# Optimization experiments

Measured on AMD Instinct MI355X. Metric: run time of the kernel, lower is better.

The kernel has to match this reference:

```python
import jax, jax.numpy as jnp
import numpy as np
from jax import lax

EPS = 1e-8

def int8_fq(x):
    # Int8ActPerTensorFloat: per-tensor float scale from runtime max-abs, fake-quant with STE.
    s = jnp.maximum(jnp.max(jnp.abs(x)) / 127.0, EPS)
    q = jnp.clip(jnp.round(x / s), -128.0, 127.0) * s
    return x + lax.stop_gradient(q - x)

def bin_w(w):
    # BINARY weight quant: per-tensor scale = mean(|w|), weights -> +/- scale (STE).
    s = jnp.mean(jnp.abs(w))
    wq = jnp.where(w >= 0, s, -s)
    return w + lax.stop_gradient(wq - w)

def qrelu(x):
    # QuantReLU with int8 input_quant and int8 act_quant
    return int8_fq(jax.nn.relu(int8_fq(x)))

def conv2d(x, w, b):
    y = lax.conv_general_dilated(x, w, window_strides=(1, 1), padding='VALID',
                                 dimension_numbers=('NCHW', 'OIHW', 'NCHW'))
    return y + b[None, :, None, None]

def maxpool2(x):
    return lax.reduce_window(x, -jnp.inf, lax.max, (1, 1, 2, 2), (1, 1, 2, 2), 'VALID')

def setup_inputs() -> dict:
    key = jax.random.key(0)
    ks = jax.random.split(key, 12)
    B = 16384
    inp = {
        'input_tensor': jax.random.normal(ks[0], (B, 3, 32, 32), dtype=jnp.float32),
        'w1': jax.random.normal(ks[1], (6, 3, 5, 5), dtype=jnp.float32) * 0.1,
        'b1': jax.random.normal(ks[2], (6,), dtype=jnp.float32) * 0.01,
        'w2': jax.random.normal(ks[3], (16, 6, 5, 5), dtype=jnp.float32) * 0.1,
        'b2': jax.random.normal(ks[4], (16,), dtype=jnp.float32) * 0.01,
        'fw1': jax.random.normal(ks[5], (120, 400), dtype=jnp.float32) * 0.05,
        'fb1': jax.random.normal(ks[6], (120,), dtype=jnp.float32) * 0.01,
        'fw2': jax.random.normal(ks[7], (84, 120), dtype=jnp.float32) * 0.05,
        'fb2': jax.random.normal(ks[8], (84,), dtype=jnp.float32) * 0.01,
        'fw3': jax.random.normal(ks[9], (10, 84), dtype=jnp.float32) * 0.05,
        'fb3': jax.random.normal(ks[10], (10,), dtype=jnp.float32) * 0.01,
    }
    return inp

def reference(input_tensor, w1, b1, w2, b2, fw1, fb1, fw2, fb2, fw3, fb3):
    x = int8_fq(input_tensor)                  # QuantIdentity
    x = qrelu(conv2d(x, bin_w(w1), b1))        # conv1 + relu1: [B,6,28,28]
    x = maxpool2(x)                            # [B,6,14,14]
    x = qrelu(conv2d(x, bin_w(w2), b2))        # conv2 + relu2: [B,16,10,10]
    x = maxpool2(x)                            # [B,16,5,5]
    x = x.reshape(x.shape[0], -1)              # [B,400]
    x = qrelu(x @ bin_w(fw1).T + fb1)          # fc1 + relu3: [B,120]
    x = qrelu(x @ bin_w(fw2).T + fb2)          # fc2 + relu4: [B,84]
    out = x @ bin_w(fw3).T + fb3               # fc3: [B,10]
    return out
```

## Files before the change

kernel.cpp:

```cpp
#include <hip/hip_runtime.h>
#include <math.h>

#define BATCH 16384
#define EPSQ 1e-8f

#define OFF_SCAL 0
#define OFF_WPK1 16
#define OFF_WPK2 196
#define OFF_FQ1  1156
#define OFF_FQ2  13156
#define OFF_FQ3  15844
#define OFF_A    16384
#define OFF_QIN   OFF_A
#define OFF_QC2   OFF_A
#define OFF_ISUM2 (OFF_A + 6400000)
#define OFF_QC3   (OFF_A + 10000000)
#define OFF_P3    (OFF_A + 12000000)
#define OFF_P4    (OFF_A + 14000000)
#define OFF_ISUM1 (OFF_A + 18874368)

__device__ inline int sdot4(unsigned int a, unsigned int b, int c) {
    return __builtin_amdgcn_sdot4((int)a, (int)b, c, false);
}

__device__ inline unsigned int fkey(float f) {
    unsigned int u = __float_as_uint(f);
    return (u & 0x80000000u) ? ~u : (u | 0x80000000u);
}
__device__ inline float fdec(unsigned int k) {
    unsigned int u = (k & 0x80000000u) ? (k ^ 0x80000000u) : ~k;
    return __uint_as_float(u);
}
#define KEY_ZERO   0x80000000u
#define KEY_NEGINF 0x007FFFFFu

__device__ inline float waveMax(float v) {
    #pragma unroll
    for (int off = 32; off > 0; off >>= 1)
        v = fmaxf(v, __shfl_down(v, off, 64));
    return v;
}

__device__ inline void blockAtomicMax2(float vmax, float vnmax,
                                       unsigned int* gmax, unsigned int* gnmax) {
    __shared__ float sm[4], sn[4];
    float a = waveMax(vmax), b = waveMax(vnmax);
    int tid = threadIdx.x;
    if ((tid & 63) == 0) { sm[tid >> 6] = a; sn[tid >> 6] = b; }
    __syncthreads();
    if (tid == 0) {
        atomicMax(gmax, fkey(fmaxf(fmaxf(sm[0], sm[1]), fmaxf(sm[2], sm[3]))));
        atomicMax(gnmax, fkey(fmaxf(fmaxf(sn[0], sn[1]), fmaxf(sn[2], sn[3]))));
    }
}

__device__ inline float fq_elem(float x, float s) {
    float q = fminf(fmaxf(rintf(x / s), -128.0f), 127.0f);
    return q * s;
}
__device__ inline int qrelu_code(float x, float s1, float s2) {
    float q = fq_elem(x, s1);
    q = fmaxf(q, 0.0f);
    return (int)fminf(fmaxf(rintf(q / s2), -128.0f), 127.0f);
}
__device__ inline void get_qrelu_scales(const unsigned int* scalu, int slot,
                                        float& s1, float& s2) {
    float maxa = fdec(scalu[slot]), negm = fdec(scalu[slot + 1]);
    float absm = fmaxf(maxa, negm);
    s1 = fmaxf(absm / 127.0f, EPSQ);
    float qm = fminf(fmaxf(rintf(maxa / s1), -128.0f), 127.0f) * s1;
    s2 = fmaxf(fmaxf(qm, 0.0f) / 127.0f, EPSQ);
}

__device__ inline unsigned int sgn8(float w) { return (w >= 0.0f) ? 0x01u : 0xFFu; }

__device__ inline unsigned int u32at(const unsigned int* wv, int wi, int k) {
    return (k == 0) ? wv[wi]
        : __builtin_amdgcn_perm(wv[wi + 1], wv[wi], 0x03020100u + 0x01010101u * (unsigned)k);
}

__global__ __launch_bounds__(256) void prep_kernel(const float* __restrict__ w1,
        const float* __restrict__ w2, const float* __restrict__ fw1,
        const float* __restrict__ fw2, const float* __restrict__ fw3,
        float* __restrict__ wsf) {
    int blk = blockIdx.x, tid = threadIdx.x;
    unsigned int* wsu = (unsigned int*)wsf;
    if (blk == 0) {
        if (tid == 0) wsu[0] = KEY_ZERO;
        else if (tid <= 8) wsu[tid] = KEY_NEGINF;
        return;
    }
    const float* src = nullptr; int N = 0;
    if (blk == 1)      { src = w1;  N = 450; }
    else if (blk == 2) { src = w2;  N = 2400; }
    else if (blk == 3) { src = fw1; N = 48000; }
    else if (blk == 4) { src = fw2; N = 10080; }
    else               { src = fw3; N = 840; }
    __shared__ float red[256];
    float partial = 0.0f;
    for (int i = tid; i < N; i += 256) partial += fabsf(src[i]);
    red[tid] = partial;
    __syncthreads();
    for (int s = 128; s > 0; s >>= 1) {
        if (tid < s) red[tid] += red[tid + s];
        __syncthreads();
    }
    if (tid == 0) wsf[8 + blk] = red[0] / (float)N;

    if (blk == 1) {
        for (int t = tid; t < 90; t += 256) {
            const float* wp = w1 + t * 5;
            wsu[OFF_WPK1 + 2*t] = sgn8(wp[0]) | (sgn8(wp[1])<<8) | (sgn8(wp[2])<<16) | (sgn8(wp[3])<<24);
            wsu[OFF_WPK1 + 2*t + 1] = sgn8(wp[4]) << 24;
        }
    } else if (blk == 2) {
        for (int t = tid; t < 480; t += 256) {
            const float* wp = w2 + t * 5;
            wsu[OFF_WPK2 + 2*t] = sgn8(wp[0]) | (sgn8(wp[1])<<8) | (sgn8(wp[2])<<16) | (sgn8(wp[3])<<24);
            wsu[OFF_WPK2 + 2*t + 1] = sgn8(wp[4]) << 24;
        }
    } else if (blk == 3) {
        for (int i = tid; i < 12000; i += 256) {
            int j = i / 100, k = i % 100;
            const float* wp = fw1 + j * 400 + k * 4;
            wsu[OFF_FQ1 + i] = sgn8(wp[0]) | (sgn8(wp[1])<<8) | (sgn8(wp[2])<<16) | (sgn8(wp[3])<<24);
        }
    } else if (blk == 4) {
        for (int i = tid; i < 2688; i += 256) {
            int j = i >> 5, k = i & 31;
            unsigned int u = 0;
            if (k < 30) {
                const float* wp = fw2 + j * 120 + k * 4;
                u = sgn8(wp[0]) | (sgn8(wp[1])<<8) | (sgn8(wp[2])<<16) | (sgn8(wp[3])<<24);
            }
            wsu[OFF_FQ2 + i] = u;
        }
    } else {
        for (int i = tid; i < 240; i += 256) {
            int j = i / 24, k = i % 24;
            unsigned int u = 0;
            if (k < 21) {
                const float* wp = fw3 + j * 84 + k * 4;
                u = sgn8(wp[0]) | (sgn8(wp[1])<<8) | (sgn8(wp[2])<<16) | (sgn8(wp[3])<<24);
            }
            wsu[OFF_FQ3 + i] = u;
        }
    }
}

__global__ __launch_bounds__(256) void absmax_kernel(const float4* __restrict__ x, int n4,
                                                     unsigned int* __restrict__ gkey) {
    float m = 0.0f;
    int stride = gridDim.x * 256;
    for (int i = blockIdx.x * 256 + threadIdx.x; i < n4; i += stride) {
        float4 v = x[i];
        m = fmaxf(m, fmaxf(fmaxf(fabsf(v.x), fabsf(v.y)), fmaxf(fabsf(v.z), fabsf(v.w))));
    }
    __shared__ float sm[4];
    m = waveMax(m);
    int tid = threadIdx.x;
    if ((tid & 63) == 0) sm[tid >> 6] = m;
    __syncthreads();
    if (tid == 0)
        atomicMax(gkey, fkey(fmaxf(fmaxf(sm[0], sm[1]), fmaxf(sm[2], sm[3]))));
}

__global__ __launch_bounds__(256) void quant1_kernel(const float4* __restrict__ x,
                                                     float* __restrict__ wsf) {
    unsigned int* wsu = (unsigned int*)wsf;
    float s0 = fmaxf(fdec(wsu[0]) / 127.0f, EPSQ);
    unsigned int* qin = wsu + OFF_QIN;
    int stride = gridDim.x * 256;
    const int total = BATCH * 96 * 12;
    for (int unit = blockIdx.x * 256 + threadIdx.x; unit < total; unit += stride) {
        int row_id = unit / 12, w = unit % 12;
        int plane = row_id >> 5, row = row_id & 31;
        int slot = (row >> 1) + ((row & 1) << 4);
        unsigned int u = 0;
        if (w < 8) {
            float4 v = x[row_id * 8 + w];
            int q0 = (int)fminf(fmaxf(rintf(v.x / s0), -128.f), 127.f);
            int q1 = (int)fminf(fmaxf(rintf(v.y / s0), -128.f), 127.f);
            int q2 = (int)fminf(fmaxf(rintf(v.z / s0), -128.f), 127.f);
            int q3 = (int)fminf(fmaxf(rintf(v.w / s0), -128.f), 127.f);
            u = (q0 & 255) | ((q1 & 255) << 8) | ((q2 & 255) << 16) | ((unsigned)(q3 & 255) << 24);
        }
        qin[(plane * 32 + slot) * 12 + w] = u;
    }
}

#define C1_ROWP 48
#define C1_CIS  1536
#define C1_IMGS 4608
#define C1_NIMG 8

template<int PH>
__device__ __forceinline__ void c1_phase(const unsigned char* ib, const unsigned int* wcp,
                                         int* ip, int& gmax, int& gmin) {
    int a0[14], a1[14];
    #pragma unroll
    for (int i = 0; i < 14; i++) { a0[i] = 0; a1[i] = 0; }
    #pragma unroll 1
    for (int ci = 0; ci < 3; ci++) {
        uint4 A[6]; unsigned int Bv[6];
        const unsigned char* cb = ib + ci * C1_CIS;
        #pragma unroll
        for (int r = 0; r < 6; r++) {
            const unsigned char* rb = cb + (((r & 1) << 4) + (r >> 1)) * C1_ROWP;
            if (PH == 0) {
                A[r]  = *(const uint4*)(rb);
                Bv[r] = *(const unsigned int*)(rb + 16);
            } else {
                Bv[r] = *(const unsigned int*)(rb + 12);
                A[r]  = *(const uint4*)(rb + 16);
            }
        }
        const unsigned int* wkp = wcp + ci * 10;
        unsigned int wk0[5], wk4[5];
        #pragma unroll
        for (int ky = 0; ky < 5; ky++) { wk0[ky] = wkp[2*ky]; wk4[ky] = wkp[2*ky+1]; }
        #pragma unroll
        for (int r6 = 0; r6 < 6; r6++) {
            unsigned int wq[5];
            if (PH == 0) {
                wq[0] = A[r6].x; wq[1] = A[r6].y; wq[2] = A[r6].z; wq[3] = A[r6].w; wq[4] = Bv[r6];
            } else {
                wq[0] = __builtin_amdgcn_perm(A[r6].x, Bv[r6],  0x05040302u);
                wq[1] = __builtin_amdgcn_perm(A[r6].y, A[r6].x, 0x05040302u);
                wq[2] = __builtin_amdgcn_perm(A[r6].z, A[r6].y, 0x05040302u);
                wq[3] = __builtin_amdgcn_perm(A[r6].w, A[r6].z, 0x05040302u);
                wq[4] = __builtin_amdgcn_perm(A[r6].w, A[r6].w, 0x00000302u);
            }
            unsigned int up[15];
            #pragma unroll
            for (int i = 0; i < 15; i++) up[i] = u32at(wq, i >> 2, i & 3);
            if (r6 <= 4) {
                unsigned int w0 = wk0[r6], w4 = wk4[r6];
                #pragma unroll
                for (int i = 0; i < 14; i++) {
                    a0[i] = sdot4(up[i], w0, a0[i]);
                    a0[i] = sdot4(up[i+1], w4, a0[i]);
                }
            }
            if (r6 >= 1) {
                unsigned int w0 = wk0[r6-1], w4 = wk4[r6-1];
                #pragma unroll
                for (int i = 0; i < 14; i++) {
                    a1[i] = sdot4(up[i], w0, a1[i]);
                    a1[i] = sdot4(up[i+1], w4, a1[i]);
                }
            }
        }
    }
    #pragma unroll
    for (int i = 0; i < 14; i++) {
        gmax = max(gmax, max(a0[i], a1[i]));
        gmin = min(gmin, min(a0[i], a1[i]));
    }
    #pragma unroll
    for (int p = 0; p < 7; p++)
        ip[p] = max(max(a0[2*p], a0[2*p+1]), max(a1[2*p], a1[2*p+1]));
}

__global__ __launch_bounds__(256) void conv1_kernel(const float* __restrict__ b1,
                                                    float* __restrict__ wsf) {
    __shared__ __align__(16) unsigned char xq[C1_NIMG * C1_IMGS];
    __shared__ unsigned int wpk[180];
    __shared__ float bsm[6];
    unsigned int* wsu = (unsigned int*)wsf;
    int tid = threadIdx.x;
    int b0 = blockIdx.x * C1_NIMG;
    float s0 = fmaxf(fdec(wsu[0]) / 127.0f, EPSQ);
    float seff = s0 * wsf[9];

    {
        const uint4* src = (const uint4*)((const unsigned char*)(wsu + OFF_QIN) + (size_t)b0 * C1_IMGS);
        uint4* dst = (uint4*)xq;
        for (int i = tid; i < C1_NIMG * 288; i += 256) dst[i] = src[i];
    }
    for (int i = tid; i < 180; i += 256) wpk[i] = wsu[OFF_WPK1 + i];
    if (tid < 6) bsm[tid] = b1[tid];
    __syncthreads();

    unsigned int* isum1 = wsu + OFF_ISUM1;
    float vmax = -INFINITY, vnmax = -INFINITY;
    const int ntask = C1_NIMG * 84;
    for (int t = tid; t < ntask; t += 256) {
        int img = t / 84, r = t % 84;
        int c = r / 14, py = r % 14;
        const unsigned char* ib = &xq[img * C1_IMGS + py * C1_ROWP];
        const unsigned int* wcp = &wpk[c * 30];
        int ip0[7], ip1[7];
        int gmax = -2000000000, gmin = 2000000000;
        c1_phase<0>(ib, wcp, ip0, gmax, gmin);
        c1_phase<1>(ib, wcp, ip1, gmax, gmin);
        float bias = bsm[c];
        vmax  = fmaxf(vmax,  fmaf(seff, (float)gmax, bias));
        vnmax = fmaxf(vnmax, -fmaf(seff, (float)gmin, bias));
        unsigned int* dst = isum1 + 588 * (size_t)(b0 + img) + 7 * (c * 14 + py);
        int v14[14];
        #pragma unroll
        for (int p = 0; p < 7; p++) { v14[p] = ip0[p]; v14[7 + p] = ip1[p]; }
        #pragma unroll
        for (int p = 0; p < 7; p++)
            dst[p] = (v14[2*p] & 0xFFFF) | ((unsigned)(v14[2*p+1] & 0xFFFF) << 16);
    }
    blockAtomicMax2(vmax, vnmax, wsu + 1, wsu + 2);
}

__global__ __launch_bounds__(256) void quant2_kernel(const float* __restrict__ b1,
                                                     float* __restrict__ wsf) {
    unsigned int* wsu = (unsigned int*)wsf;
    float s1, s2;
    get_qrelu_scales(wsu, 1, s1, s2);
    float s0 = fmaxf(fdec(wsu[0]) / 127.0f, EPSQ);
    float seff = s0 * wsf[9];
    float bv[6];
    #pragma unroll
    for (int c = 0; c < 6; c++) bv[c] = b1[c];
    const short* isum1 = (const short*)(wsu + OFF_ISUM1);
    unsigned int* qc2 = wsu + OFF_QC2;
    int stride = gridDim.x * 256;
    const int total = BATCH * 84 * 4;
    for (int unit = blockIdx.x * 256 + threadIdx.x; unit < total; unit += stride) {
        int row_id = unit >> 2, w = unit & 3;
        int bci = row_id / 14, row = row_id % 14;
        int ci = bci % 6;
        int slot = (row >> 1) + ((row & 1) << 3);
        float bias = bv[ci];
        unsigned int u = 0;
        const short* sp = isum1 + (size_t)bci * 196 + row * 14;
        #pragma unroll
        for (int k = 0; k < 4; k++) {
            int col = w * 4 + k;
            int code = 0;
            if (col < 14) {
                float pre = fmaf(seff, (float)sp[col], bias);
                code = qrelu_code(pre, s1, s2);
            }
            u |= ((unsigned)(code & 255)) << (8 * k);
        }
        qc2[((size_t)bci * 16 + slot) * 4 + w] = u;
    }
}

#define C2_ROWP 16
#define C2_CIS  256
#define C2_IMGS 1536
#define C2_NIMG 12

__global__ __launch_bounds__(256) void conv2_kernel(const float* __restrict__ b2,
                                                    float* __restrict__ wsf) {
    __shared__ __align__(16) unsigned char act[C2_NIMG * C2_IMGS];
    __shared__ unsigned int wpk[960];
    __shared__ float bsm[16];
    __shared__ __align__(16) short spb[C2_NIMG * 400];
    unsigned int* wsu = (unsigned int*)wsf;
    int tid = threadIdx.x;
    int b0 = blockIdx.x * C2_NIMG;
    int nimg = min(C2_NIMG, BATCH - b0);
    float s1, s2;
    get_qrelu_scales(wsu, 1, s1, s2);
    float seff = s2 * wsf[10];

    {
        const uint4* src = (const uint4*)((const unsigned char*)(wsu + OFF_QC2) + (size_t)b0 * C2_IMGS);
        uint4* dst = (uint4*)act;
        for (int i = tid; i < nimg * 96; i += 256) dst[i] = src[i];
    }
    for (int i = tid; i < 960; i += 256) wpk[i] = wsu[OFF_WPK2 + i];
    if (tid < 16) bsm[tid] = b2[tid];
    __syncthreads();

    float vmax = -INFINITY, vnmax = -INFINITY;
    int ntask = nimg * 80;
    for (int t = tid; t < ntask; t += 256) {
        int img = t / 80, r = t % 80;
        int c = r / 5, py = r % 5;
        const unsigned char* ib = &act[img * C2_IMGS + py * C2_ROWP];
        int a0[10], a1[10];
        #pragma unroll
        for (int i = 0; i < 10; i++) { a0[i] = 0; a1[i] = 0; }
        #pragma unroll 1
        for (int cig = 0; cig < 3; cig++) {
            uint4 R[2][6];
            #pragma unroll
            for (int g = 0; g < 2; g++)
                #pragma unroll
                for (int r6 = 0; r6 < 6; r6++)
                    R[g][r6] = *(const uint4*)(ib + (2*cig + g) * C2_CIS
                                + (((r6 & 1) << 3) + (r6 >> 1)) * C2_ROWP);
            #pragma unroll
            for (int g = 0; g < 2; g++) {
                int ci = 2*cig + g;
                const unsigned int* wkp = &wpk[(c * 6 + ci) * 10];
                unsigned int wk0[5], wk4[5];
                #pragma unroll
                for (int ky = 0; ky < 5; ky++) { wk0[ky] = wkp[2*ky]; wk4[ky] = wkp[2*ky+1]; }
                #pragma unroll
                for (int r6 = 0; r6 < 6; r6++) {
                    unsigned int wv[4] = { R[g][r6].x, R[g][r6].y, R[g][r6].z, R[g][r6].w };
                    unsigned int up[11];
                    #pragma unroll
                    for (int i = 0; i < 11; i++) up[i] = u32at(wv, i >> 2, i & 3);
                    if (r6 <= 4) {
                        unsigned int w0 = wk0[r6], w4 = wk4[r6];
                        #pragma unroll
                        for (int i = 0; i < 10; i++) {
                            a0[i] = sdot4(up[i], w0, a0[i]);
                            a0[i] = sdot4(up[i+1], w4, a0[i]);
                        }
                    }
                    if (r6 >= 1) {
                        unsigned int w0 = wk0[r6-1], w4 = wk4[r6-1];
                        #pragma unroll
                        for (int i = 0; i < 10; i++) {
                            a1[i] = sdot4(up[i], w0, a1[i]);
                            a1[i] = sdot4(up[i+1], w4, a1[i]);
                        }
                    }
                }
            }
        }
        int gmax = -2000000000, gmin = 2000000000;
        #pragma unroll
        for (int i = 0; i < 10; i++) {
            gmax = max(gmax, max(a0[i], a1[i]));
            gmin = min(gmin, min(a0[i], a1[i]));
        }
        float bias = bsm[c];
        vmax  = fmaxf(vmax,  fmaf(seff, (float)gmax, bias));
        vnmax = fmaxf(vnmax, -fmaf(seff, (float)gmin, bias));
        short* dst = spb + img * 400 + c * 25 + py * 5;
        #pragma unroll
        for (int p = 0; p < 5; p++)
            dst[p] = (short)max(max(a0[2*p], a0[2*p+1]), max(a1[2*p], a1[2*p+1]));
    }
    __syncthreads();
    {
        const uint4* pb4 = (const uint4*)spb;
        uint4* d4 = (uint4*)((short*)(wsu + OFF_ISUM2) + (size_t)b0 * 400);
        for (int i = tid; i < nimg * 50; i += 256) d4[i] = pb4[i];
    }
    blockAtomicMax2(vmax, vnmax, wsu + 3, wsu + 4);
}

__global__ __launch_bounds__(256) void quant3_kernel(const float* __restrict__ b2,
                                                     float* __restrict__ wsf) {
    unsigned int* wsu = (unsigned int*)wsf;
    float s1, s2;
    get_qrelu_scales(wsu, 3, s1, s2);
    float sp1, sp2;
    get_qrelu_scales(wsu, 1, sp1, sp2);
    float seff = sp2 * wsf[10];
    __shared__ float bv[16];
    if (threadIdx.x < 16) bv[threadIdx.x] = b2[threadIdx.x];
    __syncthreads();
    const short* isum2 = (const short*)(wsu + OFF_ISUM2);
    unsigned int* qc3 = wsu + OFF_QC3;
    int stride = gridDim.x * 256;
    const int total = BATCH * 100;
    for (int unit = blockIdx.x * 256 + threadIdx.x; unit < total; unit += stride) {
        int b = unit / 100, w = unit % 100;
        const short* sp = isum2 + (size_t)b * 400 + w * 4;
        unsigned int u = 0;
        #pragma unroll
        for (int k = 0; k < 4; k++) {
            int p = w * 4 + k;
            float pre = fmaf(seff, (float)sp[k], bv[p / 25]);
            int code = qrelu_code(pre, s1, s2);
            u |= ((unsigned)(code & 255)) << (8 * k);
        }
        qc3[unit] = u;
    }
}

__global__ __launch_bounds__(256) void fc1_kernel(const float* __restrict__ fb1,
                                                  float* __restrict__ wsf) {
    __shared__ unsigned int xs[32][100];
    __shared__ __align__(16) float pb[32 * 120];
    unsigned int* wsu = (unsigned int*)wsf;
    float* p3 = wsf + OFF_P3;
    int tid = threadIdx.x;
    size_t row0 = (size_t)blockIdx.x * 32;
    float s1, s2;
    get_qrelu_scales(wsu, 3, s1, s2);
    float seff = s2 * wsf[11];
    {
        const uint4* src = (const uint4*)(wsu + OFF_QC3 + row0 * 100);
        uint4* dst = (uint4*)xs;
        for (int i = tid; i < 800; i += 256) dst[i] = src[i];
    }
    __syncthreads();
    float vmax = -INFINITY, vnmax = -INFINITY;
    if (tid < 240) {
        int g = tid / 120, j = tid % 120;
        int acc[16];
        #pragma unroll
        for (int r = 0; r < 16; r++) acc[r] = 0;
        const uint4* wrow = (const uint4*)&wsu[OFF_FQ1 + j * 100];
        for (int kg = 0; kg < 25; kg++) {
            uint4 wv = wrow[kg];
            #pragma unroll
            for (int r = 0; r < 16; r++) {
                uint4 xv = *(const uint4*)&xs[g * 16 + r][kg * 4];
                acc[r] = sdot4(xv.x, wv.x, acc[r]);
                acc[r] = sdot4(xv.y, wv.y, acc[r]);
                acc[r] = sdot4(xv.z, wv.z, acc[r]);
                acc[r] = sdot4(xv.w, wv.w, acc[r]);
            }
        }
        float bias = fb1[j];
        #pragma unroll
        for (int r = 0; r < 16; r++) {
            float pv = fmaf(seff, (float)acc[r], bias);
            pb[(g * 16 + r) * 120 + j] = pv;
            vmax = fmaxf(vmax, pv); vnmax = fmaxf(vnmax, -pv);
        }
    }
    __syncthreads();
    {
        const float4* pb4 = (const float4*)pb;
        float4* d4 = (float4*)(p3 + row0 * 120);
        for (int i = tid; i < 960; i += 256) d4[i] = pb4[i];
    }
    blockAtomicMax2(vmax, vnmax, wsu + 5, wsu + 6);
}

__global__ __launch_bounds__(256) void fc2_kernel(const float* __restrict__ fb2,
                                                  float* __restrict__ wsf) {
    __shared__ unsigned int xs[48][32];
    __shared__ __align__(16) float pb[48 * 84];
    unsigned int* wsu = (unsigned int*)wsf;
    const float* p3 = wsf + OFF_P3;
    float* p4 = wsf + OFF_P4;
    int tid = threadIdx.x;
    size_t row0 = (size_t)blockIdx.x * 48;
    int nrow = min(48, (int)(BATCH - row0));
    float s1, s2;
    get_qrelu_scales(wsu, 5, s1, s2);
    float seff = s2 * wsf[12];
    const float4* src = (const float4*)(p3 + row0 * 120);
    for (int i = tid; i < nrow * 30; i += 256) {
        float4 v = src[i];
        int c0 = qrelu_code(v.x, s1, s2), c1 = qrelu_code(v.y, s1, s2);
        int c2 = qrelu_code(v.z, s1, s2), c3 = qrelu_code(v.w, s1, s2);
        xs[i / 30][i % 30] = c0 | (c1 << 8) | (c2 << 16) | ((unsigned)c3 << 24);
    }
    if (tid < 48) { xs[tid][30] = 0; xs[tid][31] = 0; }
    __syncthreads();
    float vmax = -INFINITY, vnmax = -INFINITY;
    if (tid < 252) {
        int g = tid / 84, j = tid % 84;
        int acc[16];
        #pragma unroll
        for (int r = 0; r < 16; r++) acc[r] = 0;
        const uint4* wrow = (const uint4*)&wsu[OFF_FQ2 + j * 32];
        #pragma unroll
        for (int kg = 0; kg < 8; kg++) {
            uint4 wv = wrow[kg];
            #pragma unroll
            for (int r = 0; r < 16; r++) {
                uint4 xv = *(const uint4*)&xs[g * 16 + r][kg * 4];
                acc[r] = sdot4(xv.x, wv.x, acc[r]);
                acc[r] = sdot4(xv.y, wv.y, acc[r]);
                acc[r] = sdot4(xv.z, wv.z, acc[r]);
                acc[r] = sdot4(xv.w, wv.w, acc[r]);
            }
        }
        float bias = fb2[j];
        #pragma unroll
        for (int r = 0; r < 16; r++) {
            int lr = g * 16 + r;
            if (lr < nrow) {
                float pv = fmaf(seff, (float)acc[r], bias);
                pb[lr * 84 + j] = pv;
                vmax = fmaxf(vmax, pv); vnmax = fmaxf(vnmax, -pv);
            }
        }
    }
    __syncthreads();
    {
        const float4* pb4 = (const float4*)pb;
        float4* d4 = (float4*)(p4 + row0 * 84);
        for (int i = tid; i < nrow * 21; i += 256) d4[i] = pb4[i];
    }
    blockAtomicMax2(vmax, vnmax, wsu + 7, wsu + 8);
}

__global__ __launch_bounds__(256) void fc3_kernel(const float* __restrict__ fb3,
                                                  float* __restrict__ out,
                                                  float* __restrict__ wsf) {
    __shared__ unsigned int wsm[240];
    __shared__ float bs[10];
    __shared__ __align__(16) float pb[2560];
    unsigned int* wsu = (unsigned int*)wsf;
    const float* p4 = wsf + OFF_P4;
    int tid = threadIdx.x;
    for (int i = tid; i < 240; i += 256) wsm[i] = wsu[OFF_FQ3 + i];
    if (tid < 10) bs[tid] = fb3[tid];
    __syncthreads();
    float s1, s2;
    get_qrelu_scales(wsu, 7, s1, s2);
    float seff = s2 * wsf[13];
    size_t row = (size_t)blockIdx.x * 256 + tid;
    unsigned int xr[24];
    const float4* src = (const float4*)(p4 + row * 84);
    #pragma unroll
    for (int k = 0; k < 21; k++) {
        float4 v = src[k];
        int c0 = qrelu_code(v.x, s1, s2), c1 = qrelu_code(v.y, s1, s2);
        int c2 = qrelu_code(v.z, s1, s2), c3 = qrelu_code(v.w, s1, s2);
        xr[k] = c0 | (c1 << 8) | (c2 << 16) | ((unsigned)c3 << 24);
    }
    xr[21] = 0; xr[22] = 0; xr[23] = 0;
    #pragma unroll
    for (int j = 0; j < 10; j++) {
        int acc = 0;
        #pragma unroll
        for (int k = 0; k < 24; k++) acc = sdot4(xr[k], wsm[j * 24 + k], acc);
        pb[tid * 10 + j] = fmaf(seff, (float)acc, bs[j]);
    }
    __syncthreads();
    {
        const float4* pb4 = (const float4*)pb;
        float4* d4 = (float4*)(out + (size_t)blockIdx.x * 2560);
        for (int i = tid; i < 640; i += 256) d4[i] = pb4[i];
    }
}

extern "C" void kernel_launch(void* const* d_in, const int* in_sizes, int n_in,
                              void* d_out, int out_size, void* d_ws, size_t ws_size,
                              hipStream_t stream) {
    const float* input = (const float*)d_in[0];
    const float* w1  = (const float*)d_in[1];
    const float* b1  = (const float*)d_in[2];
    const float* w2  = (const float*)d_in[3];
    const float* b2  = (const float*)d_in[4];
    const float* fw1 = (const float*)d_in[5];
    const float* fb1 = (const float*)d_in[6];
    const float* fw2 = (const float*)d_in[7];
    const float* fb2 = (const float*)d_in[8];
    const float* fw3 = (const float*)d_in[9];
    const float* fb3 = (const float*)d_in[10];
    float* ws  = (float*)d_ws;
    float* out = (float*)d_out;

    prep_kernel<<<6, 256, 0, stream>>>(w1, w2, fw1, fw2, fw3, ws);
    absmax_kernel<<<2048, 256, 0, stream>>>((const float4*)input,
                                            (int)((size_t)BATCH * 3072 / 4),
                                            (unsigned int*)ws);
    quant1_kernel<<<8192, 256, 0, stream>>>((const float4*)input, ws);
    conv1_kernel<<<BATCH / C1_NIMG, 256, 0, stream>>>(b1, ws);
    quant2_kernel<<<4096, 256, 0, stream>>>(b1, ws);
    conv2_kernel<<<(BATCH + C2_NIMG - 1) / C2_NIMG, 256, 0, stream>>>(b2, ws);
    quant3_kernel<<<2048, 256, 0, stream>>>(b2, ws);
    fc1_kernel<<<BATCH / 32, 256, 0, stream>>>(fb1, ws);
    fc2_kernel<<<(BATCH + 47) / 48, 256, 0, stream>>>(fb2, ws);
    fc3_kernel<<<BATCH / 256, 256, 0, stream>>>(fb3, out, ws);
}
```

Before: 474.0 us.

## Compute four output channels per thread in conv2 and drop perm-based shifts in conv1

The conv2 kernel now gives each thread four output channels for one pooled row, so each loaded input row and its unpacked bytes are reused across four channel accumulators instead of being reloaded per channel. This cuts LDS traffic and byte-extract work per sdot4, but raises register pressure (80 accumulators) and leaves many threads idle, since only nimg*20 tasks map onto 256 threads with no loop. Conv1's odd phase also replaces the perm-based realignment with an offset byte index into the unshifted words.

```diff
diff --git a/kernel.cpp b/kernel.cpp
--- a/kernel.cpp
+++ b/kernel.cpp
@@ -221,19 +221,19 @@
         for (int ky = 0; ky < 5; ky++) { wk0[ky] = wkp[2*ky]; wk4[ky] = wkp[2*ky+1]; }
         #pragma unroll
         for (int r6 = 0; r6 < 6; r6++) {
-            unsigned int wq[5];
+            unsigned int wv[5];
             if (PH == 0) {
-                wq[0] = A[r6].x; wq[1] = A[r6].y; wq[2] = A[r6].z; wq[3] = A[r6].w; wq[4] = Bv[r6];
+                wv[0] = A[r6].x; wv[1] = A[r6].y; wv[2] = A[r6].z; wv[3] = A[r6].w; wv[4] = Bv[r6];
             } else {
-                wq[0] = __builtin_amdgcn_perm(A[r6].x, Bv[r6],  0x05040302u);
-                wq[1] = __builtin_amdgcn_perm(A[r6].y, A[r6].x, 0x05040302u);
-                wq[2] = __builtin_amdgcn_perm(A[r6].z, A[r6].y, 0x05040302u);
-                wq[3] = __builtin_amdgcn_perm(A[r6].w, A[r6].z, 0x05040302u);
-                wq[4] = __builtin_amdgcn_perm(A[r6].w, A[r6].w, 0x00000302u);
-            }
+                wv[0] = Bv[r6]; wv[1] = A[r6].x; wv[2] = A[r6].y; wv[3] = A[r6].z; wv[4] = A[r6].w;
+            }
+            const int OFS = (PH == 0) ? 0 : 2;
             unsigned int up[15];
             #pragma unroll
-            for (int i = 0; i < 15; i++) up[i] = u32at(wq, i >> 2, i & 3);
+            for (int i = 0; i < 15; i++) {
+                int e = OFS + i;
+                up[i] = u32at(wv, e >> 2, e & 3);
+            }
             if (r6 <= 4) {
                 unsigned int w0 = wk0[r6], w4 = wk4[r6];
                 #pragma unroll
@@ -373,68 +373,68 @@
     __syncthreads();
 
     float vmax = -INFINITY, vnmax = -INFINITY;
-    int ntask = nimg * 80;
-    for (int t = tid; t < ntask; t += 256) {
-        int img = t / 80, r = t % 80;
-        int c = r / 5, py = r % 5;
+    int ntask = nimg * 20;
+    if (tid < ntask) {
+        int img = tid / 20, rem = tid % 20;
+        int cq = rem / 5, py = rem % 5;
+        int c0 = cq * 4;
         const unsigned char* ib = &act[img * C2_IMGS + py * C2_ROWP];
-        int a0[10], a1[10];
-        #pragma unroll
-        for (int i = 0; i < 10; i++) { a0[i] = 0; a1[i] = 0; }
+        int a0[4][10], a1[4][10];
+        #pragma unroll
+        for (int cc = 0; cc < 4; cc++)
+            #pragma unroll
+            for (int i = 0; i < 10; i++) { a0[cc][i] = 0; a1[cc][i] = 0; }
         #pragma unroll 1
-        for (int cig = 0; cig < 3; cig++) {
-            uint4 R[2][6];
-            #pragma unroll
-            for (int g = 0; g < 2; g++)
+        for (int ci = 0; ci < 6; ci++) {
+            uint4 R[6];
+            #pragma unroll
+            for (int r6 = 0; r6 < 6; r6++)
+                R[r6] = *(const uint4*)(ib + ci * C2_CIS + (((r6 & 1) << 3) + (r6 >> 1)) * C2_ROWP);
+            #pragma unroll
+            for (int r6 = 0; r6 < 6; r6++) {
+                unsigned int wv[4] = { R[r6].x, R[r6].y, R[r6].z, R[r6].w };
+                unsigned int up[11];
                 #pragma unroll
-                for (int r6 = 0; r6 < 6; r6++)
-                    R[g][r6] = *(const uint4*)(ib + (2*cig + g) * C2_CIS
-                                + (((r6 & 1) << 3) + (r6 >> 1)) * C2_ROWP);
-            #pragma unroll
-            for (int g = 0; g < 2; g++) {
-                int ci = 2*cig + g;
-                const unsigned int* wkp = &wpk[(c * 6 + ci) * 10];
-                unsigned int wk0[5], wk4[5];
+                for (int i = 0; i < 11; i++) up[i] = u32at(wv, i >> 2, i & 3);
                 #pragma unroll
-                for (int ky = 0; ky < 5; ky++) { wk0[ky] = wkp[2*ky]; wk4[ky] = wkp[2*ky+1]; }
-                #pragma unroll
-                for (int r6 = 0; r6 < 6; r6++) {
-                    unsigned int wv[4] = { R[g][r6].x, R[g][r6].y, R[g][r6].z, R[g][r6].w };
-                    unsigned int up[11];
-                    #pragma unroll
-                    for (int i = 0; i < 11; i++) up[i] = u32at(wv, i >> 2, i & 3);
+                for (int cc = 0; cc < 4; cc++) {
+                    const unsigned int* wkp = &wpk[((c0 + cc) * 6 + ci) * 10];
                     if (r6 <= 4) {
-                        unsigned int w0 = wk0[r6], w4 = wk4[r6];
+                        unsigned int w0 = wkp[2 * r6], w4 = wkp[2 * r6 + 1];
                         #pragma unroll
                         for (int i = 0; i < 10; i++) {
-                            a0[i] = sdot4(up[i], w0, a0[i]);
-                            a0[i] = sdot4(up[i+1], w4, a0[i]);
+                            a0[cc][i] = sdot4(up[i], w0, a0[cc][i]);
+                            a0[cc][i] = sdot4(up[i + 1], w4, a0[cc][i]);
                         }
                     }
                     if (r6 >= 1) {
-                        unsigned int w0 = wk0[r6-1], w4 = wk4[r6-1];
+                        unsigned int w0 = wkp[2 * (r6 - 1)], w4 = wkp[2 * (r6 - 1) + 1];
                         #pragma unroll
                         for (int i = 0; i < 10; i++) {
-                            a1[i] = sdot4(up[i], w0, a1[i]);
-                            a1[i] = sdot4(up[i+1], w4, a1[i]);
+                            a1[cc][i] = sdot4(up[i], w0, a1[cc][i]);
+                            a1[cc][i] = sdot4(up[i + 1], w4, a1[cc][i]);
                         }
                     }
                 }
             }
         }
-        int gmax = -2000000000, gmin = 2000000000;
-        #pragma unroll
-        for (int i = 0; i < 10; i++) {
-            gmax = max(gmax, max(a0[i], a1[i]));
-            gmin = min(gmin, min(a0[i], a1[i]));
-        }
-        float bias = bsm[c];
-        vmax  = fmaxf(vmax,  fmaf(seff, (float)gmax, bias));
-        vnmax = fmaxf(vnmax, -fmaf(seff, (float)gmin, bias));
-        short* dst = spb + img * 400 + c * 25 + py * 5;
-        #pragma unroll
-        for (int p = 0; p < 5; p++)
-            dst[p] = (short)max(max(a0[2*p], a0[2*p+1]), max(a1[2*p], a1[2*p+1]));
+        #pragma unroll
+        for (int cc = 0; cc < 4; cc++) {
+            int gmax = -2000000000, gmin = 2000000000;
+            #pragma unroll
+            for (int i = 0; i < 10; i++) {
+                gmax = max(gmax, max(a0[cc][i], a1[cc][i]));
+                gmin = min(gmin, min(a0[cc][i], a1[cc][i]));
+            }
+            float bias = bsm[c0 + cc];
+            vmax  = fmaxf(vmax,  fmaf(seff, (float)gmax, bias));
+            vnmax = fmaxf(vnmax, -fmaf(seff, (float)gmin, bias));
+            short* dst = spb + img * 400 + (c0 + cc) * 25 + py * 5;
+            #pragma unroll
+            for (int p = 0; p < 5; p++)
+                dst[p] = (short)max(max(a0[cc][2*p], a0[cc][2*p+1]),
+                                    max(a1[cc][2*p], a1[cc][2*p+1]));
+        }
     }
     __syncthreads();
     {
```

Result: no change. 470.0 us (-0.8%).
